# Kernel tuning notes

Measured on AMD Instinct MI355X. Metric: run time of the kernel, lower is better.

## Reference

```python
import jax, jax.numpy as jnp
import numpy as np

E, H = 1024, 16


def setup_inputs() -> dict:
    key = jax.random.key(0)
    k1, k2, k3, k4 = jax.random.split(key, 4)
    B, L = 4, 2048
    embeddings = jax.random.normal(k1, (B, L, E), dtype=jnp.float32)
    mask = jax.random.randint(k2, (B, L, L), 0, 2) == 1  # True = masked out
    # Params (torch Linear y = x @ W.T; we store already-transposed [in, out])
    W_qkv = jax.random.normal(k3, (E, 3 * E), dtype=jnp.float32) * 0.02
    W_out = jax.random.normal(k4, (E, E), dtype=jnp.float32) * 0.02
    return {"embeddings": embeddings, "mask": mask, "W_qkv": W_qkv, "W_out": W_out}


def reference(embeddings, mask, W_qkv, W_out):
    B, L, E_ = embeddings.shape
    A = E_ // H
    scale = A ** (-0.5)
    qkv = embeddings @ W_qkv                       # [B, L, 3E]
    qkv = qkv.reshape(B, L, H, 3 * A).transpose(0, 2, 1, 3)  # [B, H, L, 3A]
    q, k, v = jnp.split(qkv, 3, axis=-1)           # each [B, H, L, A]
    scores = jnp.einsum('bhqa,bhka->bhqk', q, k) * scale  # [B, H, L, L]
    m = mask[:, None, :, :]                        # [B, 1, L, L]
    fully = jnp.all(m, axis=-1, keepdims=True)     # rows with every key masked
    scores = jnp.where(m, -jnp.inf, scores)
    scores = jnp.where(fully, 0.0, scores)         # keep softmax finite
    attn = jax.nn.softmax(scores, axis=-1)
    attn = jnp.where(fully, 0.0, attn)             # == torch nan_to_num(0)
    values = jnp.einsum('bhqk,bhka->bhqa', attn, v)  # [B, H, L, A]
    values = values.transpose(0, 2, 1, 3).reshape(B, L, E_)
    return values @ W_out
```

## Files before the change

kernel.cpp:

```cpp
#include <hip/hip_runtime.h>
#include <hip/hip_bf16.h>

#define B_   4
#define L_   2048
#define E_   1024
#define H_   16
#define T_   8192
#define K_   1024

typedef __attribute__((ext_vector_type(8))) short bf16x8;
typedef __attribute__((ext_vector_type(4))) float f32x4;
typedef __attribute__((ext_vector_type(4))) unsigned u32x4;

#define CSC_ (0.125f * 1.44269504f)

__device__ __forceinline__ ushort f2b(float f) {
    union { float f; unsigned u; } x; x.f = f;
    unsigned r = (x.u + 0x7fffu + ((x.u >> 16) & 1u)) >> 16;
    return (ushort)r;
}

__device__ __forceinline__ float fexp2(float x) {
#if __has_builtin(__builtin_amdgcn_exp2f)
    return __builtin_amdgcn_exp2f(x);
#else
    return __expf(x * 0.69314718056f);
#endif
}

__device__ __forceinline__ unsigned pack2bf(float a, float b) {
#if __has_builtin(__builtin_amdgcn_cvt_pk_bf16_f32)
    auto t = __builtin_amdgcn_cvt_pk_bf16_f32(a, b);
    return __builtin_bit_cast(unsigned, t);
#else
    unsigned ua = __builtin_bit_cast(unsigned, a) + 0x8000u;
    unsigned ub = __builtin_bit_cast(unsigned, b) + 0x8000u;
    return __builtin_amdgcn_perm(ub, ua, 0x07060302);
#endif
}

#define GLD_LDS16(gp, lp) __builtin_amdgcn_global_load_lds( \
    (const __attribute__((address_space(1))) void*)(gp), \
    (__attribute__((address_space(3))) void*)(lp), 16, 0, 0)

__global__ void detect_mask_layout(const unsigned char* __restrict__ m, int* flag) {
    __shared__ int s;
    if (threadIdx.x == 0) s = 0;
    __syncthreads();
    int found = 0;
    for (int i = threadIdx.x; i < 4096; i += 256)
        if ((i & 3) != 0 && m[i] != 0) found = 1;
    if (found) atomicOr(&s, 1);
    __syncthreads();
    if (threadIdx.x == 0) *flag = s;
}

__global__ void pack_mask(const void* __restrict__ mraw, const int* __restrict__ flag,
                          unsigned* __restrict__ tbits) {
    int row  = blockIdx.x;
    int lane = threadIdx.x & 63;
    int wave = threadIdx.x >> 6;
    int isByte = *flag;
    int b = row >> 11, q = row & 2047;
    const unsigned char* mb = (const unsigned char*)mraw;
    const int*           mi = (const int*)mraw;
    long long base = (long long)row * L_;
    for (int w = wave; w < 32; w += 4) {
        int idx = w * 64 + lane;
        int v = isByte ? (int)mb[base + idx] : mi[base + idx];
        unsigned long long word = __ballot(v == 0);
        if (lane == 0) {
            tbits[((size_t)b * 64 + 2 * w)     * 2048 + q] = (unsigned)word;
            tbits[((size_t)b * 64 + 2 * w + 1) * 2048 + q] = (unsigned)(word >> 32);
        }
    }
}

__global__ __launch_bounds__(256) void conv_bf16(const float* __restrict__ in,
                                                 ushort* __restrict__ out) {
    int i = blockIdx.x * 256 + threadIdx.x;
    float4 v = ((const float4*)in)[i];
    uint2 o;
    o.x = (unsigned)f2b(v.x) | ((unsigned)f2b(v.y) << 16);
    o.y = (unsigned)f2b(v.z) | ((unsigned)f2b(v.w) << 16);
    ((uint2*)out)[i] = o;
}

__global__ __launch_bounds__(256) void transpose_conv(const float* __restrict__ in,
        ushort* __restrict__ out, int R, int Cn) {
    __shared__ float t[32][33];
    int c0 = blockIdx.x * 32, r0 = blockIdx.y * 32;
    int x = threadIdx.x & 31, y = threadIdx.x >> 5;
#pragma unroll
    for (int k = 0; k < 4; ++k)
        t[y + k * 8][x] = in[(size_t)(r0 + y + k * 8) * Cn + c0 + x];
    __syncthreads();
#pragma unroll
    for (int k = 0; k < 4; ++k)
        out[(size_t)(c0 + y + k * 8) * R + r0 + x] = f2b(t[x][y + k * 8]);
}

template<int NDIM, int MODE>
__global__ __launch_bounds__(256) void gemm_bf16(
        const ushort* __restrict__ Ab, const ushort* __restrict__ Bt,
        float* __restrict__ Cg, ushort* __restrict__ Qb,
        ushort* __restrict__ Kb, ushort* __restrict__ Vt) {
    __shared__ ushort As[128 * 64];
    __shared__ ushort Bs[128 * 64];
    const int tid = threadIdx.x;
    const int wv = tid >> 6, ln = tid & 63;
    const int bn = blockIdx.x * 128, bm = blockIdx.y * 128;
    const int wm = (wv & 1) * 64, wn = (wv >> 1) * 64;
    const int row16 = ln & 15, quad = ln >> 4;
    const int cg8 = (((ln & 7) ^ (ln >> 3)) * 8);

    f32x4 acc[4][4];
#pragma unroll
    for (int i = 0; i < 4; ++i)
#pragma unroll
        for (int j = 0; j < 4; ++j) acc[i][j] = (f32x4){0.f, 0.f, 0.f, 0.f};

    for (int k0 = 0; k0 < K_; k0 += 64) {
        __syncthreads();
#pragma unroll
        for (int it = 0; it < 4; ++it) {
            int rA = wv * 32 + it * 8 + (ln >> 3);
            GLD_LDS16(Ab + (size_t)(bm + rA) * K_ + k0 + cg8, &As[(wv * 32 + it * 8) * 64]);
            GLD_LDS16(Bt + (size_t)(bn + rA) * K_ + k0 + cg8, &Bs[(wv * 32 + it * 8) * 64]);
        }
        __syncthreads();
#pragma unroll
        for (int ks = 0; ks < 2; ++ks) {
            const int ch = (((ks * 4 + quad) ^ (ln & 7)) * 8);
            bf16x8 af[4], bf[4];
#pragma unroll
            for (int i = 0; i < 4; ++i)
                af[i] = *(const bf16x8*)&As[(wm + i * 16 + row16) * 64 + ch];
#pragma unroll
            for (int j = 0; j < 4; ++j)
                bf[j] = *(const bf16x8*)&Bs[(wn + j * 16 + row16) * 64 + ch];
#pragma unroll
            for (int i = 0; i < 4; ++i)
#pragma unroll
                for (int j = 0; j < 4; ++j)
                    acc[i][j] = __builtin_amdgcn_mfma_f32_16x16x32_bf16(
                        af[i], bf[j], acc[i][j], 0, 0, 0);
        }
    }

    if (MODE == 0) {
#pragma unroll
        for (int i = 0; i < 4; ++i)
#pragma unroll
            for (int j = 0; j < 4; ++j) {
                int col = bn + wn + j * 16 + row16;
#pragma unroll
                for (int r = 0; r < 4; ++r) {
                    int row = bm + wm + i * 16 + quad * 4 + r;
                    Cg[(size_t)row * NDIM + col] = acc[i][j][r];
                }
            }
    } else {
#pragma unroll
        for (int j = 0; j < 4; ++j) {
            int col = bn + wn + j * 16 + row16;
            int h = col / 192, w = col - h * 192;
            int sel = w >> 6, a = w & 63;
            float qs = (sel == 0) ? CSC_ : 1.0f;
#pragma unroll
            for (int i = 0; i < 4; ++i)
#pragma unroll
                for (int r = 0; r < 4; ++r) {
                    int rowg = bm + wm + i * 16 + quad * 4 + r;
                    int b = rowg >> 11, l = rowg & 2047;
                    ushort v = f2b(acc[i][j][r] * qs);
                    size_t bh = (size_t)(b * H_ + h);
                    if (sel == 0)      Qb[(bh * L_ + l) * 64 + a] = v;
                    else if (sel == 1) Kb[(bh * L_ + l) * 64 + a] = v;
                    else {
                        int k5 = l & 31;
                        int lp = (l & ~31) | (2 * (k5 & 15) + (k5 >> 4));
                        Vt[(bh * 64 + a) * L_ + lp] = v;
                    }
                }
        }
    }
}

__global__ __launch_bounds__(512, 4) void attn_mfma(
        const ushort* __restrict__ Qb, const ushort* __restrict__ Kb,
        const ushort* __restrict__ Vt, const unsigned* __restrict__ tbits,
        ushort* __restrict__ vals) {
    __shared__ ushort KV[6][2048];

    const int tid = threadIdx.x, wv = tid >> 6, ln = tid & 63;
    const int bh = blockIdx.y, b = bh >> 4, h = bh & 15;
    const int q0 = blockIdx.x * 128;
    const int row16 = ln & 15, quad = ln >> 4;
    const int lh = ln >> 3, ll = ln & 7;
    const int cg8 = ((ll ^ lh) * 8);

    const ushort* Kg = Kb + (size_t)bh * L_ * 64;
    const ushort* Vg = Vt + (size_t)bh * 64 * L_;

    const int wk = wv & 3;
    const bool isK = (wv < 4);
    const int vc4 = ll ^ lh;
    const ushort* vsrc = Vg + (size_t)(wk * 8 + lh + 32 * (vc4 >> 2)) * L_ + (vc4 & 3) * 8;
    const ushort* ksrc = Kg + (size_t)(wk * 8 + lh) * 64 + cg8;

    {
        const ushort* Qgw = Qb + ((size_t)bh * L_ + q0 + wv * 16) * 64;
        GLD_LDS16(Qgw + (size_t)lh * 64 + cg8,       &KV[0][(wv * 16) * 64]);
        GLD_LDS16(Qgw + (size_t)(8 + lh) * 64 + cg8, &KV[0][(wv * 16 + 8) * 64]);
    }
    __syncthreads();
    bf16x8 aq[2];
#pragma unroll
    for (int ks = 0; ks < 2; ++ks)
        aq[ks] = *(const bf16x8*)&KV[0][(wv * 16 + row16) * 64 +
                                        (((ks * 4 + quad) ^ (row16 & 7)) * 8)];
    __syncthreads();

    if (isK) {
        GLD_LDS16(ksrc,        &KV[0][(wk * 8) * 64]);
        GLD_LDS16(ksrc + 2048, &KV[1][(wk * 8) * 64]);
    } else {
        GLD_LDS16(vsrc,        &KV[3][(wk * 8) * 64]);
        GLD_LDS16(vsrc + 32,   &KV[4][(wk * 8) * 64]);
    }

    ushort *kc = KV[0], *kn = KV[1], *kf = KV[2];
    ushort *vcb = KV[3], *vnb = KV[4], *vfb = KV[5];
    const ushort* kstage = ksrc + 2 * 2048;
    const ushort* vstage = vsrc + 2 * 32;

    bf16x8 vone;
#pragma unroll
    for (int i = 0; i < 8; ++i) vone[i] = (short)0x3F80;

    f32x4 oacc[4], lacc = (f32x4){0.f, 0.f, 0.f, 0.f};
#pragma unroll
    for (int t = 0; t < 4; ++t) oacc[t] = (f32x4){0.f, 0.f, 0.f, 0.f};

    const unsigned* mptr = tbits + (size_t)b * 64 * 2048 + (q0 + wv * 16 + row16);

    auto qk = [&](const ushort* kbuf, f32x4 (&s)[2]) {
#pragma unroll
        for (int t = 0; t < 2; ++t) s[t] = (f32x4){0.f, 0.f, 0.f, 0.f};
        __builtin_amdgcn_s_setprio(1);
#pragma unroll
        for (int ks = 0; ks < 2; ++ks) {
            bf16x8 bk[2];
#pragma unroll
            for (int t = 0; t < 2; ++t)
                bk[t] = *(const bf16x8*)&kbuf[(t * 16 + row16) * 64 +
                                              (((ks * 4 + quad) ^ (row16 & 7)) * 8)];
#pragma unroll
            for (int t = 0; t < 2; ++t)
                s[t] = __builtin_amdgcn_mfma_f32_16x16x32_bf16(
                    bk[t], aq[ks], s[t], 0, 0, 0);
        }
        __builtin_amdgcn_s_setprio(0);
    };

    auto softmax_pv = [&](f32x4 (&sa)[2], unsigned m) {
        u32x4 pw;
#pragma unroll
        for (int r = 0; r < 4; ++r) {
            unsigned sh = m >> (quad * 4 + r);
            unsigned pk = pack2bf(fexp2(sa[0][r]), fexp2(sa[1][r]));
            pk &= (sh & 0x00010001u) * 0xFFFFu;
            pw[r] = pk;
        }
        bf16x8 ap = __builtin_bit_cast(bf16x8, pw);
        bf16x8 bv[4];
#pragma unroll
        for (int t = 0; t < 4; ++t)
            bv[t] = *(const bf16x8*)&vcb[((t & 1) * 16 + row16) * 64 +
                                         ((((t >> 1) * 4 + quad) ^ (row16 & 7)) * 8)];
        __builtin_amdgcn_s_setprio(1);
        lacc = __builtin_amdgcn_mfma_f32_16x16x32_bf16(ap, vone, lacc, 0, 0, 0);
#pragma unroll
        for (int t = 0; t < 4; ++t)
            oacc[t] = __builtin_amdgcn_mfma_f32_16x16x32_bf16(
                ap, bv[t], oacc[t], 0, 0, 0);
        __builtin_amdgcn_s_setprio(0);
    };

    auto body = [&](bool do_stage, f32x4 (&sa)[2], f32x4 (&sn)[2],
                    unsigned &mc, unsigned &mn) {
        mn = *mptr;
        mptr += 2048;
        if (do_stage) {
            if (isK) { GLD_LDS16(kstage, &kf[(wk * 8) * 64]);  kstage += 2048; }
            else     { GLD_LDS16(vstage, &vfb[(wk * 8) * 64]); vstage += 32; }
        }
        qk(kn, sn);
        softmax_pv(sa, mc);
        __syncthreads();
        ushort* t;
        t = kc;  kc  = kn;  kn  = kf;  kf  = t;
        t = vcb; vcb = vnb; vnb = vfb; vfb = t;
    };

    unsigned mA, mB;
    mA = *mptr;
    mptr += 2048;
    f32x4 sA[2], sB[2];
    __syncthreads();
    qk(kc, sA);

    for (int i = 0; i < 31; ++i) {
        body(true, sA, sB, mA, mB);
        body(2 * i + 1 < 62, sB, sA, mB, mA);
    }
    body(false, sA, sB, mA, mB);
    softmax_pv(sB, mB);

#pragma unroll
    for (int r = 0; r < 4; ++r) {
        float l = lacc[r];
        float inv = (l > 0.f) ? 1.0f / l : 0.f;
        int qrow = q0 + wv * 16 + quad * 4 + r;
        size_t base = ((size_t)b * L_ + qrow) * E_ + h * 64;
#pragma unroll
        for (int t = 0; t < 4; ++t)
            vals[base + t * 16 + row16] = f2b(oacc[t][r] * inv);
    }
}

extern "C" void kernel_launch(void* const* d_in, const int* in_sizes, int n_in,
                              void* d_out, int out_size, void* d_ws, size_t ws_size,
                              hipStream_t stream) {
    const float* emb  = (const float*)d_in[0];
    const void*  mask = d_in[1];
    const float* wqkv = (const float*)d_in[2];
    const float* wout = (const float*)d_in[3];
    float* out = (float*)d_out;

    char* ws = (char*)d_ws;
    const size_t NEED = 4096ull + 2097152ull + 2ull * 46137344ull;
    if (ws_size < NEED) return;

    int* flag = (int*)ws;
    unsigned* tbits = (unsigned*)(ws + 4096);
    ushort* embb  = (ushort*)(ws + 4096 + 2097152);
    ushort* Wqkvt = embb  + 8388608;
    ushort* Wott  = Wqkvt + 3145728;
    ushort* Qb    = Wott  + 1048576;
    ushort* Kb    = Qb    + 8388608;
    ushort* Vt    = Kb    + 8388608;
    ushort* vals  = Vt    + 8388608;

    detect_mask_layout<<<1, 256, 0, stream>>>((const unsigned char*)mask, flag);
    pack_mask<<<T_, 256, 0, stream>>>(mask, flag, tbits);
    conv_bf16<<<8192, 256, 0, stream>>>(emb, embb);
    transpose_conv<<<dim3(96, 32), 256, 0, stream>>>(wqkv, Wqkvt, 1024, 3072);
    transpose_conv<<<dim3(32, 32), 256, 0, stream>>>(wout, Wott, 1024, 1024);
    gemm_bf16<3072, 1><<<dim3(24, 64), 256, 0, stream>>>(
        embb, Wqkvt, nullptr, Qb, Kb, Vt);
    attn_mfma<<<dim3(16, 64), 512, 0, stream>>>(Qb, Kb, Vt, tbits, vals);
    gemm_bf16<1024, 0><<<dim3(8, 64), 256, 0, stream>>>(
        vals, Wott, out, nullptr, nullptr, nullptr);
}
```

Measured before the change: 365.0 us.

## Switch attention KV pipeline to double-buffered 64-key tiles

Replaces the triple-buffered 32-key K/V ring, which overlapped QK of the next tile with softmax-PV of the current one, with double-buffered 64-key tiles processed as two 32-key halves per iteration. This halves the number of __syncthreads barriers and loop iterations and loads mask words for both halves up front. The cost is that QK and PV are no longer software-pipelined across iterations, so MFMA latency may be exposed. Only one tile of prefetch distance remains to hide global loads.

```diff
diff --git a/kernel.cpp b/kernel.cpp
--- a/kernel.cpp
+++ b/kernel.cpp
@@ -191,7 +191,7 @@
         const ushort* __restrict__ Qb, const ushort* __restrict__ Kb,
         const ushort* __restrict__ Vt, const unsigned* __restrict__ tbits,
         ushort* __restrict__ vals) {
-    __shared__ ushort KV[6][2048];
+    __shared__ ushort KV[4][4096];
 
     const int tid = threadIdx.x, wv = tid >> 6, ln = tid & 63;
     const int bh = blockIdx.y, b = bh >> 4, h = bh & 15;
@@ -206,8 +206,8 @@
     const int wk = wv & 3;
     const bool isK = (wv < 4);
     const int vc4 = ll ^ lh;
-    const ushort* vsrc = Vg + (size_t)(wk * 8 + lh + 32 * (vc4 >> 2)) * L_ + (vc4 & 3) * 8;
-    const ushort* ksrc = Kg + (size_t)(wk * 8 + lh) * 64 + cg8;
+    const ushort* vstage = Vg + (size_t)(wk * 8 + lh + 32 * (vc4 >> 2)) * L_ + (vc4 & 3) * 8;
+    const ushort* kstage = Kg + (size_t)(wk * 8 + lh) * 64 + cg8;
 
     {
         const ushort* Qgw = Qb + ((size_t)bh * L_ + q0 + wv * 16) * 64;
@@ -223,48 +223,43 @@
     __syncthreads();
 
     if (isK) {
-        GLD_LDS16(ksrc,        &KV[0][(wk * 8) * 64]);
-        GLD_LDS16(ksrc + 2048, &KV[1][(wk * 8) * 64]);
+        GLD_LDS16(kstage,        &KV[0][(wk * 8) * 64]);
+        GLD_LDS16(kstage + 2048, &KV[0][(32 + wk * 8) * 64]);
     } else {
-        GLD_LDS16(vsrc,        &KV[3][(wk * 8) * 64]);
-        GLD_LDS16(vsrc + 32,   &KV[4][(wk * 8) * 64]);
-    }
-
-    ushort *kc = KV[0], *kn = KV[1], *kf = KV[2];
-    ushort *vcb = KV[3], *vnb = KV[4], *vfb = KV[5];
-    const ushort* kstage = ksrc + 2 * 2048;
-    const ushort* vstage = vsrc + 2 * 32;
+        GLD_LDS16(vstage,      &KV[2][(wk * 8) * 64]);
+        GLD_LDS16(vstage + 32, &KV[2][(32 + wk * 8) * 64]);
+    }
+    kstage += 4096; vstage += 64;
 
     bf16x8 vone;
 #pragma unroll
     for (int i = 0; i < 8; ++i) vone[i] = (short)0x3F80;
-
-    f32x4 oacc[4], lacc = (f32x4){0.f, 0.f, 0.f, 0.f};
-#pragma unroll
-    for (int t = 0; t < 4; ++t) oacc[t] = (f32x4){0.f, 0.f, 0.f, 0.f};
+    const f32x4 zf = (f32x4){0.f, 0.f, 0.f, 0.f};
+
+    f32x4 oacc[4], lacc = zf;
+#pragma unroll
+    for (int t = 0; t < 4; ++t) oacc[t] = zf;
 
     const unsigned* mptr = tbits + (size_t)b * 64 * 2048 + (q0 + wv * 16 + row16);
 
-    auto qk = [&](const ushort* kbuf, f32x4 (&s)[2]) {
-#pragma unroll
-        for (int t = 0; t < 2; ++t) s[t] = (f32x4){0.f, 0.f, 0.f, 0.f};
+    auto qk = [&](const ushort* kbuf, int sub, f32x4 (&s)[2]) {
         __builtin_amdgcn_s_setprio(1);
 #pragma unroll
         for (int ks = 0; ks < 2; ++ks) {
             bf16x8 bk[2];
 #pragma unroll
             for (int t = 0; t < 2; ++t)
-                bk[t] = *(const bf16x8*)&kbuf[(t * 16 + row16) * 64 +
+                bk[t] = *(const bf16x8*)&kbuf[(sub * 32 + t * 16 + row16) * 64 +
                                               (((ks * 4 + quad) ^ (row16 & 7)) * 8)];
 #pragma unroll
             for (int t = 0; t < 2; ++t)
                 s[t] = __builtin_amdgcn_mfma_f32_16x16x32_bf16(
-                    bk[t], aq[ks], s[t], 0, 0, 0);
+                    bk[t], aq[ks], ks ? s[t] : zf, 0, 0, 0);
         }
         __builtin_amdgcn_s_setprio(0);
     };
 
-    auto softmax_pv = [&](f32x4 (&sa)[2], unsigned m) {
+    auto sm_pv = [&](f32x4 (&sa)[2], unsigned m, const ushort* vbuf, int sub) {
         u32x4 pw;
 #pragma unroll
         for (int r = 0; r < 4; ++r) {
@@ -277,8 +272,8 @@
         bf16x8 bv[4];
 #pragma unroll
         for (int t = 0; t < 4; ++t)
-            bv[t] = *(const bf16x8*)&vcb[((t & 1) * 16 + row16) * 64 +
-                                         ((((t >> 1) * 4 + quad) ^ (row16 & 7)) * 8)];
+            bv[t] = *(const bf16x8*)&vbuf[(sub * 32 + (t & 1) * 16 + row16) * 64 +
+                                          ((((t >> 1) * 4 + quad) ^ (row16 & 7)) * 8)];
         __builtin_amdgcn_s_setprio(1);
         lacc = __builtin_amdgcn_mfma_f32_16x16x32_bf16(ap, vone, lacc, 0, 0, 0);
 #pragma unroll
@@ -288,35 +283,37 @@
         __builtin_amdgcn_s_setprio(0);
     };
 
-    auto body = [&](bool do_stage, f32x4 (&sa)[2], f32x4 (&sn)[2],
-                    unsigned &mc, unsigned &mn) {
-        mn = *mptr;
-        mptr += 2048;
-        if (do_stage) {
-            if (isK) { GLD_LDS16(kstage, &kf[(wk * 8) * 64]);  kstage += 2048; }
-            else     { GLD_LDS16(vstage, &vfb[(wk * 8) * 64]); vstage += 32; }
-        }
-        qk(kn, sn);
-        softmax_pv(sa, mc);
+    auto iter = [&](const ushort* kb, const ushort* vb,
+                    ushort* kn, ushort* vn, bool st) {
+        unsigned m0 = mptr[0], m1 = mptr[2048];
+        mptr += 4096;
+        if (st) {
+            if (isK) {
+                GLD_LDS16(kstage,        kn + (wk * 8) * 64);
+                GLD_LDS16(kstage + 2048, kn + (32 + wk * 8) * 64);
+                kstage += 4096;
+            } else {
+                GLD_LDS16(vstage,      vn + (wk * 8) * 64);
+                GLD_LDS16(vstage + 32, vn + (32 + wk * 8) * 64);
+                vstage += 64;
+            }
+        }
+        f32x4 s0[2], s1[2];
+        qk(kb, 0, s0);
+        qk(kb, 1, s1);
+        sm_pv(s0, m0, vb, 0);
+        sm_pv(s1, m1, vb, 1);
         __syncthreads();
-        ushort* t;
-        t = kc;  kc  = kn;  kn  = kf;  kf  = t;
-        t = vcb; vcb = vnb; vnb = vfb; vfb = t;
     };
 
-    unsigned mA, mB;
-    mA = *mptr;
-    mptr += 2048;
-    f32x4 sA[2], sB[2];
-    __syncthreads();
-    qk(kc, sA);
-
-    for (int i = 0; i < 31; ++i) {
-        body(true, sA, sB, mA, mB);
-        body(2 * i + 1 < 62, sB, sA, mB, mA);
-    }
-    body(false, sA, sB, mA, mB);
-    softmax_pv(sB, mB);
+    __syncthreads();
+
+    for (int i = 0; i < 15; ++i) {
+        iter(KV[0], KV[2], KV[1], KV[3], true);
+        iter(KV[1], KV[3], KV[0], KV[2], true);
+    }
+    iter(KV[0], KV[2], KV[1], KV[3], true);
+    iter(KV[1], KV[3], KV[0], KV[2], false);
 
 #pragma unroll
     for (int r = 0; r < 4; ++r) {
```

Measured after the change: 357.9 us. No clear change (-1.9%).
